# Optimization experiments

Measured on AMD Instinct MI355X. Metric: run time of the kernel, lower is better.

## Reference

```python
import jax, jax.numpy as jnp
import numpy as np

B, T = 4, 1024
V = 1024          # vocab_size (tied to block_size via weight tying)
BLK = 1024        # block_size
C = 768           # n_embd
H = 12            # n_head
HS = C // H       # head_size = 64
L = 6             # n_layer
F = 4 * C         # FFN hidden
STD = 0.02
EPS = 1e-5


def layer_norm(x, w, b):
    m = x.mean(-1, keepdims=True)
    v = ((x - m) ** 2).mean(-1, keepdims=True)
    return (x - m) / jnp.sqrt(v + EPS) * w + b


def setup_inputs() -> dict:
    key = jax.random.key(0)
    ks = jax.random.split(key, 12)
    n = lambda k, shape: jax.random.normal(k, shape, dtype=jnp.float32) * STD
    inp = {
        "idx": jax.random.randint(ks[0], (B, T), 0, V),
        "targets": jax.random.randint(ks[1], (B, T), 0, V),
        "wte": n(ks[2], (V, C)),            # tied with lm_head weight
        "wpe": n(ks[3], (BLK, C)),
        "lm_b": jnp.zeros((V,), jnp.float32),
        "ln1_w": jnp.ones((L, C), jnp.float32),
        "ln1_b": jnp.zeros((L, C), jnp.float32),
        "Wq": n(ks[4], (L, C, C)),           # per-layer stacked head projections (head-major columns)
        "Wk": n(ks[5], (L, C, C)),
        "Wv": n(ks[6], (L, C, C)),
        "proj_W": n(ks[7], (L, C, C)),
        "proj_b": jnp.zeros((L, C), jnp.float32),
        "ln2_w": jnp.ones((L, C), jnp.float32),
        "ln2_b": jnp.zeros((L, C), jnp.float32),
        "fc1_W": n(ks[8], (L, C, F)),
        "fc1_b": jnp.zeros((L, F), jnp.float32),
        "fc2_W": n(ks[9], (L, F, C)),
        "fc2_b": jnp.zeros((L, C), jnp.float32),
        "lnf_w": jnp.ones((C,), jnp.float32),
        "lnf_b": jnp.zeros((C,), jnp.float32),
    }
    return inp


def reference(idx, targets, wte, wpe, lm_b, ln1_w, ln1_b, Wq, Wk, Wv,
              proj_W, proj_b, ln2_w, ln2_b, fc1_W, fc1_b, fc2_W, fc2_b,
              lnf_w, lnf_b):
    Bc, Tc = idx.shape
    x = wte[idx] + wpe[jnp.arange(Tc)]          # [B,T,C]
    mask = jnp.tril(jnp.ones((Tc, Tc), bool))   # causal tril buffer
    neg_inf = jnp.asarray(-jnp.inf, x.dtype)
    for l in range(L):
        h = layer_norm(x, ln1_w[l], ln1_b[l])
        q = (h @ Wq[l]).reshape(Bc, Tc, H, HS)
        k = (h @ Wk[l]).reshape(Bc, Tc, H, HS)
        v = (h @ Wv[l]).reshape(Bc, Tc, H, HS)
        wei = jnp.einsum('bqhd,bkhd->bhqk', q, k) * (HS ** -0.5)
        wei = jnp.where(mask, wei, neg_inf)
        wei = jax.nn.softmax(wei, axis=-1)
        att = jnp.einsum('bhqk,bkhd->bqhd', wei, v).reshape(Bc, Tc, C)
        x = att @ proj_W[l] + proj_b[l] + x
        h2 = layer_norm(x, ln2_w[l], ln2_b[l])
        x = jax.nn.relu(h2 @ fc1_W[l] + fc1_b[l]) @ fc2_W[l] + fc2_b[l] + x
    x = layer_norm(x, lnf_w, lnf_b)
    logits = x @ wte.T + lm_b                   # weight-tied lm_head
    logp = jax.nn.log_softmax(logits, axis=-1)
    loss = -jnp.take_along_axis(logp, targets[..., None], axis=-1).mean()
    return logits, loss
```

## Files before the change

### kernel.cpp

```cpp
#include <hip/hip_runtime.h>
#include <hip/hip_bf16.h>

typedef short bf16x8 __attribute__((ext_vector_type(8)));
typedef unsigned short u16x8 __attribute__((ext_vector_type(8)));
typedef float f32x4 __attribute__((ext_vector_type(4)));

#define B_ 4
#define T_ 1024
#define V_ 1024
#define C_ 768
#define H_ 12
#define HS_ 64
#define L_ 6
#define F_ 3072
#define M_ (B_ * T_)
#define QKV_ 2304

__device__ inline float b2f(unsigned short u) {
    return __uint_as_float(((unsigned int)u) << 16);
}
__device__ inline unsigned short f2bbits(float f) {
    __hip_bfloat16 h = __float2bfloat16(f);
    return *(unsigned short*)&h;
}
__device__ inline void load_lds_16(const void* g, void* l) {
    __builtin_amdgcn_global_load_lds(
        (const __attribute__((address_space(1))) unsigned int*)g,
        (__attribute__((address_space(3))) unsigned int*)l, 16, 0, 0);
}

__global__ void convert_bf16_kernel(const float* __restrict__ in,
                                    __hip_bfloat16* __restrict__ out, int n) {
    int i = blockIdx.x * 256 + threadIdx.x;
    if (i < n) out[i] = __float2bfloat16(in[i]);
}

__global__ void embed_kernel(const int* __restrict__ idx,
                             const float* __restrict__ wte,
                             const float* __restrict__ wpe,
                             __hip_bfloat16* __restrict__ x) {
    int i = blockIdx.x * 256 + threadIdx.x;
    int row = i / C_;
    int c = i - row * C_;
    int t = row & (T_ - 1);
    x[i] = __float2bfloat16(wte[(size_t)idx[row] * C_ + c] + wpe[(size_t)t * C_ + c]);
}

__global__ __launch_bounds__(256) void ln4_kernel(const __hip_bfloat16* __restrict__ x,
                                                  const float* __restrict__ w,
                                                  const float* __restrict__ b,
                                                  __hip_bfloat16* __restrict__ out) {
    int row = blockIdx.x * 4 + (threadIdx.x >> 6);
    int lane = threadIdx.x & 63;
    const unsigned short* xr = (const unsigned short*)x + (size_t)row * C_;
    float v[12];
    float s = 0.0f;
    #pragma unroll
    for (int j = 0; j < 12; j++) { v[j] = b2f(xr[lane + 64 * j]); s += v[j]; }
    #pragma unroll
    for (int o = 32; o; o >>= 1) s += __shfl_xor(s, o);
    float mean = s * (1.0f / C_);
    float vs = 0.0f;
    #pragma unroll
    for (int j = 0; j < 12; j++) { v[j] -= mean; vs += v[j] * v[j]; }
    #pragma unroll
    for (int o = 32; o; o >>= 1) vs += __shfl_xor(vs, o);
    float rstd = rsqrtf(vs * (1.0f / C_) + 1e-5f);
    __hip_bfloat16* o = out + (size_t)row * C_;
    #pragma unroll
    for (int j = 0; j < 12; j++) {
        int c = lane + 64 * j;
        o[c] = __float2bfloat16(v[j] * rstd * w[c] + b[c]);
    }
}

__global__ void transpose_bf16_kernel(const float* __restrict__ W,
                                      __hip_bfloat16* __restrict__ WT,
                                      int K, int N,
                                      size_t sStride, size_t dStride) {
    int l = blockIdx.z;
    W += (size_t)l * sStride;
    WT += (size_t)l * dStride;
    __shared__ float tile[32][33];
    int n0 = blockIdx.x * 32, k0 = blockIdx.y * 32;
    int tx = threadIdx.x, ty = threadIdx.y;
    #pragma unroll
    for (int i = 0; i < 4; i++)
        tile[ty + 8 * i][tx] = W[(size_t)(k0 + ty + 8 * i) * N + n0 + tx];
    __syncthreads();
    #pragma unroll
    for (int i = 0; i < 4; i++)
        WT[(size_t)(n0 + ty + 8 * i) * K + k0 + tx] =
            __float2bfloat16(tile[tx][ty + 8 * i]);
}

__global__ void transpose_qkv_kernel(const float* __restrict__ Wq,
                                     const float* __restrict__ Wk,
                                     const float* __restrict__ Wv,
                                     __hip_bfloat16* __restrict__ dst) {
    int z = blockIdx.z;
    int l = z / 3, which = z % 3;
    const float* W = (which == 0 ? Wq : which == 1 ? Wk : Wv) + (size_t)l * C_ * C_;
    __hip_bfloat16* WT = dst + (size_t)l * QKV_ * C_ + (size_t)which * C_ * C_;
    __shared__ float tile[32][33];
    int n0 = blockIdx.x * 32, k0 = blockIdx.y * 32;
    int tx = threadIdx.x, ty = threadIdx.y;
    #pragma unroll
    for (int i = 0; i < 4; i++)
        tile[ty + 8 * i][tx] = W[(size_t)(k0 + ty + 8 * i) * C_ + n0 + tx];
    __syncthreads();
    #pragma unroll
    for (int i = 0; i < 4; i++)
        WT[(size_t)(n0 + ty + 8 * i) * C_ + k0 + tx] =
            __float2bfloat16(tile[tx][ty + 8 * i]);
}

template <int BN, int DEPTH, bool BIAS, bool RES, bool RELU, bool OUTF, bool OUTB>
__global__ __launch_bounds__(256) void gemm64xN_kernel(
    const __hip_bfloat16* __restrict__ A,
    const __hip_bfloat16* __restrict__ WT,
    const float* __restrict__ bias,
    const __hip_bfloat16* __restrict__ res,
    float* __restrict__ outF,
    __hip_bfloat16* __restrict__ outB,
    int M, int N, int K, int nbx) {
    constexpr int BJ = BN / 32;
    __shared__ __align__(16) short As[DEPTH * 64 * 64];
    __shared__ __align__(16) short Bs[DEPTH * BN * 64];
    int tid = threadIdx.x;
    int lane = tid & 63;
    int w = tid >> 6;
    int l15 = lane & 15, l4 = lane >> 4;

    int nwg = gridDim.x;
    int bid = blockIdx.x;
    int sbid = (bid & 7) * (nwg >> 3) + (bid >> 3);
    int bx = sbid % nbx, by = sbid / nbx;
    int row0 = by * 64, col0 = bx * BN;

    int wr = w >> 1, wc = w & 1;

    int rr = tid >> 3;
    int cswz = (((tid & 7) ^ (rr & 7)) * 8);
    const char* Ag = (const char*)A + ((size_t)(row0 + rr) * K + cswz) * 2;
    const char* Bg = (const char*)WT + ((size_t)(col0 + rr) * K + cswz) * 2;

    f32x4 acc[2][BJ] = {};
    int ktiles = K >> 6;

    auto stage = [&](int buf, int k0) {
        const char* Agk = Ag + (size_t)k0 * 2;
        const char* Bgk = Bg + (size_t)k0 * 2;
        #pragma unroll
        for (int i = 0; i < 2; i++)
            load_lds_16(Agk + (size_t)i * 32 * K * 2,
                        (char*)As + buf * 8192 + i * 4096 + w * 1024);
        #pragma unroll
        for (int i = 0; i < BN / 32; i++)
            load_lds_16(Bgk + (size_t)i * 32 * K * 2,
                        (char*)Bs + buf * (BN * 128) + i * 4096 + w * 1024);
    };

    stage(0, 0);
    if (DEPTH == 3 && ktiles > 1) stage(1, 64);
    int rxor = (l15 & 7) << 4;
    for (int t = 0; t < ktiles; ++t) {
        if constexpr (DEPTH == 2) {
            if (t + 1 < ktiles) {
                stage((t + 1) & 1, (t + 1) * 64);
                if constexpr (BN == 128)
                    asm volatile("s_waitcnt vmcnt(6)" ::: "memory");
                else
                    asm volatile("s_waitcnt vmcnt(4)" ::: "memory");
            } else {
                asm volatile("s_waitcnt vmcnt(0)" ::: "memory");
            }
        } else {
            if (t + 2 < ktiles) {
                stage((t + 2) % 3, (t + 2) * 64);
                asm volatile("s_waitcnt vmcnt(8)" ::: "memory");
            } else if (t + 1 < ktiles) {
                asm volatile("s_waitcnt vmcnt(4)" ::: "memory");
            } else {
                asm volatile("s_waitcnt vmcnt(0)" ::: "memory");
            }
        }
        __builtin_amdgcn_s_barrier();
        asm volatile("" ::: "memory");
        int cur = (DEPTH == 2) ? (t & 1) : (t % 3);
        const char* Asb = (const char*)As + cur * 8192;
        const char* Bsb = (const char*)Bs + cur * (BN * 128);
        #pragma unroll
        for (int kk = 0; kk < 2; kk++) {
            bf16x8 a[2], b[BJ];
            #pragma unroll
            for (int i = 0; i < 2; i++)
                a[i] = *(const bf16x8*)(Asb +
                        (wr * 32 + i * 16 + l15) * 128 + ((kk * 64 + l4 * 16) ^ rxor));
            #pragma unroll
            for (int j = 0; j < BJ; j++)
                b[j] = *(const bf16x8*)(Bsb +
                        (wc * (BN / 2) + j * 16 + l15) * 128 + ((kk * 64 + l4 * 16) ^ rxor));
            #pragma unroll
            for (int i = 0; i < 2; i++)
                #pragma unroll
                for (int j = 0; j < BJ; j++)
                    acc[i][j] = __builtin_amdgcn_mfma_f32_16x16x32_bf16(
                        a[i], b[j], acc[i][j], 0, 0, 0);
        }
        asm volatile("" ::: "memory");
        __builtin_amdgcn_s_barrier();
    }

    int rbase = l4 * 4;
    #pragma unroll
    for (int i = 0; i < 2; i++) {
        #pragma unroll
        for (int j = 0; j < BJ; j++) {
            int col = col0 + wc * (BN / 2) + j * 16 + l15;
            float bv = BIAS ? bias[col] : 0.0f;
            #pragma unroll
            for (int r = 0; r < 4; r++) {
                int row = row0 + wr * 32 + i * 16 + rbase + r;
                size_t off = (size_t)row * N + col;
                float v = acc[i][j][r] + bv;
                if (RES) v += b2f(((const unsigned short*)res)[off]);
                if (RELU) v = fmaxf(v, 0.0f);
                if (OUTF) outF[off] = v;
                if (OUTB) outB[off] = __float2bfloat16(v);
            }
        }
    }
}

__global__ __launch_bounds__(512) void attn_flash_kernel(
    const __hip_bfloat16* __restrict__ qkvb,
    __hip_bfloat16* __restrict__ attb) {
    int tid = threadIdx.x;
    int lane = tid & 63;
    int w = tid >> 6;
    int l15 = lane & 15;
    int l4 = lane >> 4;

    int bid = blockIdx.x;
    int xcd = bid & 7, i = bid >> 3;
    int qc = 7 - (i / 6);
    int bh = (i % 6) * 8 + xcd;
    int b = bh / H_, h = bh % H_;
    int qb0 = qc * 128;

    __shared__ __align__(16) unsigned short Ks[2][128 * 64];
    __shared__ __align__(16) unsigned short Vt[2][64 * 128];
    __shared__ __align__(16) unsigned short Ps[8 * 16 * 64];

    const unsigned short* qkv = (const unsigned short*)qkvb;
    const unsigned short* Qg = qkv + (size_t)(b * T_ + qb0) * QKV_ + h * HS_;
    const unsigned short* Kg = qkv + (size_t)b * T_ * QKV_ + C_ + h * HS_;
    const unsigned short* Vg = qkv + (size_t)b * T_ * QKV_ + 2 * C_ + h * HS_;

    bf16x8 qfrag[2];
    {
        const short* qrow = (const short*)Qg + (size_t)(w * 16 + l15) * QKV_;
        qfrag[0] = *(const bf16x8*)(qrow + l4 * 8);
        qfrag[1] = *(const bf16x8*)(qrow + 32 + l4 * 8);
    }

    f32x4 o_acc[4] = {};
    float l_part[4] = {0.0f, 0.0f, 0.0f, 0.0f};

    unsigned short* Pw = Ps + w * 16 * 64;
    int nkb128 = qc + 1;
    const float CS = 0.18033688f;

    int key = tid >> 3, ch = tid & 7;
    int kbyte0 = key * 128 + ((ch * 16) ^ ((key & 7) << 4));
    int kbyte1 = (key + 64) * 128 + ((ch * 16) ^ ((key & 7) << 4));

    auto vt_write = [&](unsigned short* dst, int half, const u16x8& vv) {
        #pragma unroll
        for (int e = 0; e < 8; ++e) {
            int d = ch * 8 + e;
            int slot = (d ^ (d >> 3)) & 7;
            *(unsigned short*)((char*)dst + d * 256 + half * 128 +
                               ((key * 2) ^ (slot << 4))) = (unsigned short)vv[e];
        }
    };

    u16x8 kreg0 = *(const u16x8*)(Kg + (size_t)key * QKV_ + ch * 8);
    u16x8 kreg1 = *(const u16x8*)(Kg + (size_t)(key + 64) * QKV_ + ch * 8);
    u16x8 vreg0 = *(const u16x8*)(Vg + (size_t)key * QKV_ + ch * 8);
    u16x8 vreg1 = *(const u16x8*)(Vg + (size_t)(key + 64) * QKV_ + ch * 8);
    *(u16x8*)((char*)Ks[0] + kbyte0) = kreg0;
    *(u16x8*)((char*)Ks[0] + kbyte1) = kreg1;
    vt_write(Vt[0], 0, vreg0);
    vt_write(Vt[0], 1, vreg1);

    int cur = 0;
    for (int kbi = 0; kbi < nkb128; ++kbi) {
        int k0 = kbi * 128;
        __syncthreads();
        bool pref = (kbi + 1 < nkb128);
        if (pref) {
            kreg0 = *(const u16x8*)(Kg + (size_t)(k0 + 128 + key) * QKV_ + ch * 8);
            kreg1 = *(const u16x8*)(Kg + (size_t)(k0 + 192 + key) * QKV_ + ch * 8);
            vreg0 = *(const u16x8*)(Vg + (size_t)(k0 + 128 + key) * QKV_ + ch * 8);
            vreg1 = *(const u16x8*)(Vg + (size_t)(k0 + 192 + key) * QKV_ + ch * 8);
        }

        #pragma unroll
        for (int half = 0; half < 2; ++half) {
            f32x4 s[4] = {};
            __builtin_amdgcn_s_setprio(1);
            #pragma unroll
            for (int kk = 0; kk < 2; ++kk) {
                #pragma unroll
                for (int nt = 0; nt < 4; ++nt) {
                    int kyf = half * 64 + nt * 16 + l15;
                    int boff = kyf * 128 + (((l4 * 16) + kk * 64) ^ ((kyf & 7) << 4));
                    bf16x8 kf = *(const bf16x8*)((char*)Ks[cur] + boff);
                    s[nt] = __builtin_amdgcn_mfma_f32_16x16x32_bf16(
                        qfrag[kk], kf, s[nt], 0, 0, 0);
                }
            }
            __builtin_amdgcn_s_setprio(0);

            bool maskt = (kbi * 2 + half >= 2 * qc);
            #pragma unroll
            for (int nt = 0; nt < 4; ++nt)
                #pragma unroll
                for (int r = 0; r < 4; ++r) {
                    float v = s[nt][r] * CS;
                    if (maskt) {
                        int ky = k0 + half * 64 + nt * 16 + l15;
                        int q = qb0 + w * 16 + l4 * 4 + r;
                        if (ky > q) v = -1e30f;
                    }
                    s[nt][r] = exp2f(v);
                }
            #pragma unroll
            for (int r = 0; r < 4; ++r)
                l_part[r] += (s[0][r] + s[1][r]) + (s[2][r] + s[3][r]);

            #pragma unroll
            for (int nt = 0; nt < 4; ++nt)
                #pragma unroll
                for (int r = 0; r < 4; ++r) {
                    int q = l4 * 4 + r;
                    int col = nt * 16 + l15;
                    int boff = q * 128 + ((col * 2) ^ ((q & 7) << 4));
                    *(unsigned short*)((char*)Pw + boff) = f2bbits(s[nt][r]);
                }

            __builtin_amdgcn_s_setprio(1);
            #pragma unroll
            for (int kk = 0; kk < 2; ++kk) {
                int q = l15;
                int pboff = q * 128 + (((l4 * 16) + kk * 64) ^ ((q & 7) << 4));
                bf16x8 pf = *(const bf16x8*)((char*)Pw + pboff);
                #pragma unroll
                for (int nt = 0; nt < 4; ++nt) {
                    int d = nt * 16 + l15;
                    int dslot = (d ^ (d >> 3)) & 7;
                    int vboff = d * 256 + half * 128 +
                                (((l4 * 16) + kk * 64) ^ (dslot << 4));
                    bf16x8 vf = *(const bf16x8*)((char*)Vt[cur] + vboff);
                    o_acc[nt] = __builtin_amdgcn_mfma_f32_16x16x32_bf16(
                        pf, vf, o_acc[nt], 0, 0, 0);
                }
            }
            __builtin_amdgcn_s_setprio(0);
        }

        if (pref) {
            *(u16x8*)((char*)Ks[cur ^ 1] + kbyte0) = kreg0;
            *(u16x8*)((char*)Ks[cur ^ 1] + kbyte1) = kreg1;
            vt_write(Vt[cur ^ 1], 0, vreg0);
            vt_write(Vt[cur ^ 1], 1, vreg1);
        }
        cur ^= 1;
    }

    #pragma unroll
    for (int r = 0; r < 4; ++r) {
        #pragma unroll
        for (int o = 8; o; o >>= 1) l_part[r] += __shfl_xor(l_part[r], o);
    }
    unsigned short* Og = (unsigned short*)attb + (size_t)(b * T_ + qb0) * C_ + h * HS_;
    #pragma unroll
    for (int r = 0; r < 4; ++r) {
        float inv = 1.0f / l_part[r];
        #pragma unroll
        for (int nt = 0; nt < 4; ++nt) {
            float val = o_acc[nt][r] * inv;
            Og[(size_t)(w * 16 + l4 * 4 + r) * C_ + nt * 16 + l15] = f2bbits(val);
        }
    }
}

__global__ void loss_rows_kernel(const float* __restrict__ logits,
                                 const int* __restrict__ targets,
                                 float* __restrict__ partials) {
    int row = blockIdx.x, tid = threadIdx.x;
    const float* lr = logits + (size_t)row * V_;
    __shared__ float red[256];
    float sum = 0.0f;
    for (int i = tid; i < V_; i += 256) sum += __expf(lr[i]);
    red[tid] = sum;
    __syncthreads();
    for (int s = 128; s; s >>= 1) {
        if (tid < s) red[tid] += red[tid + s];
        __syncthreads();
    }
    if (tid == 0)
        partials[row] = __logf(red[0]) - lr[targets[row]];
}

__global__ void loss_reduce_kernel(const float* __restrict__ partials,
                                   float* __restrict__ out) {
    int tid = threadIdx.x;
    float s = 0.0f;
    for (int i = tid; i < M_; i += 256) s += partials[i];
    __shared__ float red[256];
    red[tid] = s;
    __syncthreads();
    for (int st = 128; st; st >>= 1) {
        if (tid < st) red[tid] += red[tid + st];
        __syncthreads();
    }
    if (tid == 0) out[0] = red[0] * (1.0f / M_);
}

extern "C" void kernel_launch(void* const* d_in, const int* in_sizes, int n_in,
                              void* d_out, int out_size, void* d_ws, size_t ws_size,
                              hipStream_t stream) {
    const int*   idx     = (const int*)d_in[0];
    const int*   targets = (const int*)d_in[1];
    const float* wte     = (const float*)d_in[2];
    const float* wpe     = (const float*)d_in[3];
    const float* lm_b    = (const float*)d_in[4];
    const float* ln1_w   = (const float*)d_in[5];
    const float* ln1_b   = (const float*)d_in[6];
    const float* Wq      = (const float*)d_in[7];
    const float* Wk      = (const float*)d_in[8];
    const float* Wv      = (const float*)d_in[9];
    const float* projW   = (const float*)d_in[10];
    const float* projb   = (const float*)d_in[11];
    const float* ln2_w   = (const float*)d_in[12];
    const float* ln2_b   = (const float*)d_in[13];
    const float* fc1W    = (const float*)d_in[14];
    const float* fc1b    = (const float*)d_in[15];
    const float* fc2W    = (const float*)d_in[16];
    const float* fc2b    = (const float*)d_in[17];
    const float* lnfw    = (const float*)d_in[18];
    const float* lnfb    = (const float*)d_in[19];

    char* ws = (char*)d_ws;
    size_t off = 0;
    __hip_bfloat16* x    = (__hip_bfloat16*)(ws + off); off += (size_t)M_ * C_ * 2;
    __hip_bfloat16* h    = (__hip_bfloat16*)(ws + off); off += (size_t)M_ * C_ * 2;
    size_t qkv_off = off;
    __hip_bfloat16* qkvb = (__hip_bfloat16*)(ws + off); off += (size_t)M_ * QKV_ * 2;
    __hip_bfloat16* attb = (__hip_bfloat16*)(ws + off); off += (size_t)M_ * C_ * 2;
    __hip_bfloat16* fb   = (__hip_bfloat16*)(ws + qkv_off);
    __hip_bfloat16* wteB = (__hip_bfloat16*)(ws + off); off += (size_t)V_ * C_ * 2;
    float* partials = (float*)(ws + off);          off += (size_t)M_ * 4;

    const size_t QKV_SZ = (size_t)QKV_ * C_;
    const size_t WP_SZ  = (size_t)C_ * C_;
    const size_t F1_SZ  = (size_t)C_ * F_;
    const size_t F2_SZ  = (size_t)F_ * C_;
    size_t upfront_bytes = off + 2 * (size_t)L_ * (QKV_SZ + WP_SZ + F1_SZ + F2_SZ);
    bool upfront = ws_size >= upfront_bytes;
    int rep = upfront ? L_ : 1;

    __hip_bfloat16* qkvT0 = (__hip_bfloat16*)(ws + off); off += 2 * (size_t)rep * QKV_SZ;
    __hip_bfloat16* wpT0  = (__hip_bfloat16*)(ws + off); off += 2 * (size_t)rep * WP_SZ;
    __hip_bfloat16* wf1T0 = (__hip_bfloat16*)(ws + off); off += 2 * (size_t)rep * F1_SZ;
    __hip_bfloat16* wf2T0 = (__hip_bfloat16*)(ws + off); off += 2 * (size_t)rep * F2_SZ;

    float* logits = (float*)d_out;
    float* loss   = (float*)d_out + (size_t)M_ * V_;

    convert_bf16_kernel<<<(V_ * C_ + 255) / 256, 256, 0, stream>>>(wte, wteB, V_ * C_);
    embed_kernel<<<(M_ * C_) / 256, 256, 0, stream>>>(idx, wte, wpe, x);

    if (upfront) {
        transpose_qkv_kernel<<<dim3(C_ / 32, C_ / 32, 3 * L_), dim3(32, 8), 0, stream>>>(
            Wq, Wk, Wv, qkvT0);
        transpose_bf16_kernel<<<dim3(C_ / 32, C_ / 32, L_), dim3(32, 8), 0, stream>>>(
            projW, wpT0, C_, C_, WP_SZ, WP_SZ);
        transpose_bf16_kernel<<<dim3(F_ / 32, C_ / 32, L_), dim3(32, 8), 0, stream>>>(
            fc1W, wf1T0, C_, F_, F1_SZ, F1_SZ);
        transpose_bf16_kernel<<<dim3(C_ / 32, F_ / 32, L_), dim3(32, 8), 0, stream>>>(
            fc2W, wf2T0, F_, C_, F2_SZ, F2_SZ);
    }

    for (int l = 0; l < L_; l++) {
        __hip_bfloat16* qkvT = qkvT0 + (upfront ? (size_t)l * QKV_SZ : 0);
        __hip_bfloat16* wpT  = wpT0  + (upfront ? (size_t)l * WP_SZ : 0);
        __hip_bfloat16* wf1T = wf1T0 + (upfront ? (size_t)l * F1_SZ : 0);
        __hip_bfloat16* wf2T = wf2T0 + (upfront ? (size_t)l * F2_SZ : 0);

        ln4_kernel<<<M_ / 4, 256, 0, stream>>>(x, ln1_w + l * C_, ln1_b + l * C_, h);

        if (!upfront)
            transpose_qkv_kernel<<<dim3(C_ / 32, C_ / 32, 3), dim3(32, 8), 0, stream>>>(
                Wq + (size_t)l * C_ * C_, Wk + (size_t)l * C_ * C_,
                Wv + (size_t)l * C_ * C_, qkvT);

        gemm64xN_kernel<128, 2, false, false, false, false, true>
            <<<(M_ / 64) * (QKV_ / 128), 256, 0, stream>>>(
            h, qkvT, nullptr, nullptr, nullptr, qkvb, M_, QKV_, C_, QKV_ / 128);

        attn_flash_kernel<<<B_ * H_ * (T_ / 128), 512, 0, stream>>>(qkvb, attb);

        if (!upfront)
            transpose_bf16_kernel<<<dim3(C_ / 32, C_ / 32, 1), dim3(32, 8), 0, stream>>>(
                projW + (size_t)l * C_ * C_, wpT, C_, C_, 0, 0);
        gemm64xN_kernel<64, 3, true, true, false, false, true>
            <<<(M_ / 64) * (C_ / 64), 256, 0, stream>>>(
            attb, wpT, projb + l * C_, x, nullptr, x, M_, C_, C_, C_ / 64);

        ln4_kernel<<<M_ / 4, 256, 0, stream>>>(x, ln2_w + l * C_, ln2_b + l * C_, h);

        if (!upfront)
            transpose_bf16_kernel<<<dim3(F_ / 32, C_ / 32, 1), dim3(32, 8), 0, stream>>>(
                fc1W + (size_t)l * C_ * F_, wf1T, C_, F_, 0, 0);
        gemm64xN_kernel<128, 2, true, false, true, false, true>
            <<<(M_ / 64) * (F_ / 128), 256, 0, stream>>>(
            h, wf1T, fc1b + l * F_, nullptr, nullptr, fb, M_, F_, C_, F_ / 128);

        if (!upfront)
            transpose_bf16_kernel<<<dim3(C_ / 32, F_ / 32, 1), dim3(32, 8), 0, stream>>>(
                fc2W + (size_t)l * F_ * C_, wf2T, F_, C_, 0, 0);
        gemm64xN_kernel<64, 3, true, true, false, false, true>
            <<<(M_ / 64) * (C_ / 64), 256, 0, stream>>>(
            fb, wf2T, fc2b + l * C_, x, nullptr, x, M_, C_, F_, C_ / 64);
    }

    ln4_kernel<<<M_ / 4, 256, 0, stream>>>(x, lnfw, lnfb, h);
    gemm64xN_kernel<128, 2, true, false, false, true, false>
        <<<(M_ / 64) * (V_ / 128), 256, 0, stream>>>(
        h, wteB, lm_b, nullptr, logits, nullptr, M_, V_, C_, V_ / 128);

    loss_rows_kernel<<<M_, 256, 0, stream>>>(logits, targets, partials);
    loss_reduce_kernel<<<1, 256, 0, stream>>>(partials, loss);
}
```

Baseline: 902.1 us.

## Vectorize embedding and loss rows; switch QKV/FC1/LM GEMMs to 64-wide tiles

```diff
diff --git a/kernel.cpp b/kernel.cpp
--- a/kernel.cpp
+++ b/kernel.cpp
@@ -39,11 +39,20 @@
                              const float* __restrict__ wte,
                              const float* __restrict__ wpe,
                              __hip_bfloat16* __restrict__ x) {
-    int i = blockIdx.x * 256 + threadIdx.x;
-    int row = i / C_;
-    int c = i - row * C_;
+    int i4 = blockIdx.x * 256 + threadIdx.x;
+    int row = i4 / (C_ / 4);
+    int c4 = i4 - row * (C_ / 4);
     int t = row & (T_ - 1);
-    x[i] = __float2bfloat16(wte[(size_t)idx[row] * C_ + c] + wpe[(size_t)t * C_ + c]);
+    float4 we = ((const float4*)wte)[(size_t)idx[row] * (C_ / 4) + c4];
+    float4 wp = ((const float4*)wpe)[(size_t)t * (C_ / 4) + c4];
+    u16x8 o8;
+    unsigned short o[4];
+    o[0] = f2bbits(we.x + wp.x);
+    o[1] = f2bbits(we.y + wp.y);
+    o[2] = f2bbits(we.z + wp.z);
+    o[3] = f2bbits(we.w + wp.w);
+    *(ushort1*)&o8 = *(ushort1*)o;
+    *((ushort4*)((unsigned short*)x + (size_t)i4 * 4)) = *(ushort4*)o;
 }
 
 __global__ __launch_bounds__(256) void ln4_kernel(const __hip_bfloat16* __restrict__ x,
@@ -397,22 +406,23 @@
     }
 }
 
-__global__ void loss_rows_kernel(const float* __restrict__ logits,
-                                 const int* __restrict__ targets,
-                                 float* __restrict__ partials) {
-    int row = blockIdx.x, tid = threadIdx.x;
-    const float* lr = logits + (size_t)row * V_;
-    __shared__ float red[256];
+__global__ __launch_bounds__(256) void loss_rows_kernel(
+    const float* __restrict__ logits,
+    const int* __restrict__ targets,
+    float* __restrict__ partials) {
+    int row = blockIdx.x * 4 + (threadIdx.x >> 6);
+    int lane = threadIdx.x & 63;
+    const float4* lr = (const float4*)(logits + (size_t)row * V_);
     float sum = 0.0f;
-    for (int i = tid; i < V_; i += 256) sum += __expf(lr[i]);
-    red[tid] = sum;
-    __syncthreads();
-    for (int s = 128; s; s >>= 1) {
-        if (tid < s) red[tid] += red[tid + s];
-        __syncthreads();
-    }
-    if (tid == 0)
-        partials[row] = __logf(red[0]) - lr[targets[row]];
+    #pragma unroll
+    for (int j = 0; j < 4; j++) {
+        float4 v = lr[lane + 64 * j];
+        sum += __expf(v.x) + __expf(v.y) + __expf(v.z) + __expf(v.w);
+    }
+    #pragma unroll
+    for (int o = 32; o; o >>= 1) sum += __shfl_xor(sum, o);
+    if (lane == 0)
+        partials[row] = __logf(sum) - logits[(size_t)row * V_ + targets[row]];
 }
 
 __global__ void loss_reduce_kernel(const float* __restrict__ partials,
@@ -482,7 +492,7 @@
     float* loss   = (float*)d_out + (size_t)M_ * V_;
 
     convert_bf16_kernel<<<(V_ * C_ + 255) / 256, 256, 0, stream>>>(wte, wteB, V_ * C_);
-    embed_kernel<<<(M_ * C_) / 256, 256, 0, stream>>>(idx, wte, wpe, x);
+    embed_kernel<<<(M_ * C_ / 4) / 256, 256, 0, stream>>>(idx, wte, wpe, x);
 
     if (upfront) {
         transpose_qkv_kernel<<<dim3(C_ / 32, C_ / 32, 3 * L_), dim3(32, 8), 0, stream>>>(
@@ -508,9 +518,9 @@
                 Wq + (size_t)l * C_ * C_, Wk + (size_t)l * C_ * C_,
                 Wv + (size_t)l * C_ * C_, qkvT);
 
-        gemm64xN_kernel<128, 2, false, false, false, false, true>
-            <<<(M_ / 64) * (QKV_ / 128), 256, 0, stream>>>(
-            h, qkvT, nullptr, nullptr, nullptr, qkvb, M_, QKV_, C_, QKV_ / 128);
+        gemm64xN_kernel<64, 3, false, false, false, false, true>
+            <<<(M_ / 64) * (QKV_ / 64), 256, 0, stream>>>(
+            h, qkvT, nullptr, nullptr, nullptr, qkvb, M_, QKV_, C_, QKV_ / 64);
 
         attn_flash_kernel<<<B_ * H_ * (T_ / 128), 512, 0, stream>>>(qkvb, attb);
 
@@ -526,9 +536,9 @@
         if (!upfront)
             transpose_bf16_kernel<<<dim3(F_ / 32, C_ / 32, 1), dim3(32, 8), 0, stream>>>(
                 fc1W + (size_t)l * C_ * F_, wf1T, C_, F_, 0, 0);
-        gemm64xN_kernel<128, 2, true, false, true, false, true>
-            <<<(M_ / 64) * (F_ / 128), 256, 0, stream>>>(
-            h, wf1T, fc1b + l * F_, nullptr, nullptr, fb, M_, F_, C_, F_ / 128);
+        gemm64xN_kernel<64, 3, true, false, true, false, true>
+            <<<(M_ / 64) * (F_ / 64), 256, 0, stream>>>(
+            h, wf1T, fc1b + l * F_, nullptr, nullptr, fb, M_, F_, C_, F_ / 64);
 
         if (!upfront)
             transpose_bf16_kernel<<<dim3(C_ / 32, F_ / 32, 1), dim3(32, 8), 0, stream>>>(
@@ -539,10 +549,10 @@
     }
 
     ln4_kernel<<<M_ / 4, 256, 0, stream>>>(x, lnfw, lnfb, h);
-    gemm64xN_kernel<128, 2, true, false, false, true, false>
-        <<<(M_ / 64) * (V_ / 128), 256, 0, stream>>>(
-        h, wteB, lm_b, nullptr, logits, nullptr, M_, V_, C_, V_ / 128);
-
-    loss_rows_kernel<<<M_, 256, 0, stream>>>(logits, targets, partials);
+    gemm64xN_kernel<64, 3, true, false, false, true, false>
+        <<<(M_ / 64) * (V_ / 64), 256, 0, stream>>>(
+        h, wteB, lm_b, nullptr, logits, nullptr, M_, V_, C_, V_ / 64);
+
+    loss_rows_kernel<<<M_ / 4, 256, 0, stream>>>(logits, targets, partials);
     loss_reduce_kernel<<<1, 256, 0, stream>>>(partials, loss);
 }
```

Result: slower. 980.5 us (+8.7%).
